# Kernel optimization log

Hardware: AMD Instinct MI355X
Metric: run time of the kernel (lower is better)

## Reference

```python
import jax, jax.numpy as jnp
import numpy as np

BITWIDTH = 8  # args.actBitwidth


def setup_inputs() -> dict:
    key = jax.random.key(0)
    k1, k2, k3 = jax.random.split(key, 3)
    x = jax.random.normal(k1, (32, 256, 56, 56), dtype=jnp.float32)
    # orthonormal-ish projection matrix (stand-in for PCA eigenvectors)
    u = jax.random.normal(k2, (256, 256), dtype=jnp.float32) / np.float32(np.sqrt(256.0))
    # positive per-channel clamp values
    clamp_val = jax.random.uniform(k3, (256,), dtype=jnp.float32) * 3.0 + 0.5
    return {"x": x, "u": u, "clamp_val": clamp_val}


def reference(x, u, clamp_val):
    N, C, H, W = x.shape
    x = jax.nn.relu(x)
    # [C, N*H*W] channel-major flatten (matches transpose(0,1).view(C,-1))
    im = jnp.transpose(x, (1, 0, 2, 3)).reshape(C, -1)
    mn = jnp.mean(im, axis=1, keepdims=True)
    im = im - mn
    # PCA projection
    p = u.T @ im  # [C, NHW]
    # per-channel symmetric clamp
    c = clamp_val[:, None]
    pq = jnp.clip(p, -c, c)
    # per-channel dynamic min/max uniform quantization (fused over channels)
    dmax = jnp.max(pq, axis=1, keepdims=True)
    dmin = jnp.min(pq, axis=1, keepdims=True)
    rng = dmax - dmin
    scale = (2.0 ** BITWIDTH - 1.0) / jnp.where(rng == 0, 1.0, rng)
    q = jnp.round((pq - dmin) * scale) / scale + dmin
    q = jnp.where(rng == 0, pq, q)
    # project back, re-center, add channel means
    out = u @ q
    out = out - jnp.mean(out, axis=1, keepdims=True) + mn
    return jnp.transpose(out.reshape(C, N, H, W), (1, 0, 2, 3))
```

## Files before the change

### kernel.cpp

```cpp
#include <hip/hip_runtime.h>
#include <hip/hip_bf16.h>
#include <stdint.h>

#define CH    256
#define HWsz  3136
#define NIMG  32
#define COLS  (NIMG * HWsz)
#define KB    32
#define TN    64
#define TILES (COLS / TN)
#define PBLK  2
#define NBINS 8
#define CHUNK (TN * 20)

typedef float  f32x4  __attribute__((ext_vector_type(4)));
typedef __bf16 bf16x8 __attribute__((ext_vector_type(8)));

struct Stats {
  float mnsum[NBINS][CH];
  float mn[CH];
  float poff[CH];
  float clF[CH];
  unsigned dminK[NBINS][CH];
  unsigned dmaxK[NBINS][CH];
  float dminF[CH];
  float scaleF[CH];
  float invF[CH];
  float qsum[CH];
  float corr[CH];
  unsigned short u_bf[CH * CH];
  unsigned short uT_bf[CH * CH];
};

__device__ __forceinline__ unsigned short f2bf(float f) {
  union { float f; unsigned u; } v; v.f = f;
  unsigned r = v.u + 0x7fffu + ((v.u >> 16) & 1u);
  return (unsigned short)(r >> 16);
}
__device__ __forceinline__ float bf2f(unsigned short b) {
  union { unsigned u; float f; } v; v.u = ((unsigned)b) << 16;
  return v.f;
}
__device__ __forceinline__ unsigned pack_bf2(float a, float b) {
  return (unsigned)f2bf(a) | ((unsigned)f2bf(b) << 16);
}
__device__ __forceinline__ unsigned fkey(float f) {
  unsigned u = __float_as_uint(f);
  return (u & 0x80000000u) ? ~u : (u | 0x80000000u);
}
__device__ __forceinline__ float funkey(unsigned k) {
  unsigned u = (k & 0x80000000u) ? (k & 0x7fffffffu) : ~k;
  return __uint_as_float(u);
}
__device__ __forceinline__ float clampf(float v, float c) {
  return fminf(fmaxf(v, -c), c);
}
__device__ __forceinline__ float dq(float v, float dmin, float sc, float inv) {
  return sc == 0.f ? v : fmaf(rintf((v - dmin) * sc), inv, dmin);
}

__global__ void k_init(const float* __restrict__ u, Stats* st) {
  int b = blockIdx.x, t = threadIdx.x;
  st->u_bf[b * CH + t]  = f2bf(u[b * CH + t]);
  st->uT_bf[b * CH + t] = f2bf(u[t * CH + b]);
  if (b < NBINS) {
    st->mnsum[b][t] = 0.f;
    st->dminK[b][t] = 0xFFFFFFFFu;
    st->dmaxK[b][t] = 0u;
  }
  if (b == 0) st->qsum[t] = 0.f;
}

__global__ __launch_bounds__(256) void k_gemm1(const float* __restrict__ x,
                                               Stats* __restrict__ st,
                                               unsigned* __restrict__ pq,
                                               long nstride) {
  __shared__ __align__(16) unsigned ldsU[8 * CHUNK];
  __shared__ float smin[CH];
  __shared__ float smax[CH];

  const int t = threadIdx.x;
  const int lane = t & 63, wv = t >> 6;
  const int g = t & 15, cpair = t >> 4;
  const int c2 = cpair & 3;
  const int q = lane >> 4, r15 = lane & 15;
  const int wsw = (((wv ^ ((g >> 1) & 3)) << 2) | c2);

  const int t0 = blockIdx.x * PBLK;
  const unsigned short* uT = st->uT_bf;

  smin[t] = 1e30f;
  smax[t] = -1e30f;

  f32x4 acc[4][4] = {};
  float4 rA[8], rB[8];
  float relp[8][2] = {};

  auto ldtile = [&](int tile) {
    const int n = tile / 49, hw0 = (tile % 49) * TN;
    const float* p0 = x + (size_t)n * CH * HWsz + (size_t)(2 * cpair) * HWsz + hw0 + 4 * g;
#pragma unroll
    for (int kc = 0; kc < 8; ++kc) {
      const float* p = p0 + (size_t)(kc * KB) * HWsz;
      rA[kc] = *(const float4*)p;
      rB[kc] = *(const float4*)(p + HWsz);
    }
  };
  auto stageall = [&]() {
#pragma unroll
    for (int kc = 0; kc < 8; ++kc) {
      const float a[4] = {fmaxf(rA[kc].x, 0.f), fmaxf(rA[kc].y, 0.f),
                          fmaxf(rA[kc].z, 0.f), fmaxf(rA[kc].w, 0.f)};
      const float b[4] = {fmaxf(rB[kc].x, 0.f), fmaxf(rB[kc].y, 0.f),
                          fmaxf(rB[kc].z, 0.f), fmaxf(rB[kc].w, 0.f)};
      relp[kc][0] += (a[0] + a[1]) + (a[2] + a[3]);
      relp[kc][1] += (b[0] + b[1]) + (b[2] + b[3]);
      unsigned* dst = ldsU + kc * CHUNK;
#pragma unroll
      for (int i = 0; i < 4; ++i)
        dst[(4 * g + i) * 20 + wsw] = pack_bf2(a[i], b[i]);
    }
  };
  auto epi = [&](int tile) {
    const int n = tile / 49, hw0 = (tile % 49) * TN;
#pragma unroll
    for (int mt = 0; mt < 4; ++mt) {
      const int kp0 = 32 * wv + 8 * mt + 2 * q;
      float mn4[4], mx4[4];
#pragma unroll
      for (int nt = 0; nt < 4; ++nt) {
        const unsigned w01 = pack_bf2(acc[mt][nt][0], acc[mt][nt][1]);
        const unsigned w23 = pack_bf2(acc[mt][nt][2], acc[mt][nt][3]);
        const size_t base = (size_t)n * nstride + (size_t)kp0 * HWsz + hw0 + nt * 16 + r15;
        pq[base]        = w01;
        pq[base + HWsz] = w23;
        const float v[4] = {bf2f((unsigned short)(w01 & 0xffffu)), bf2f((unsigned short)(w01 >> 16)),
                            bf2f((unsigned short)(w23 & 0xffffu)), bf2f((unsigned short)(w23 >> 16))};
#pragma unroll
        for (int reg = 0; reg < 4; ++reg) {
          if (nt == 0) { mn4[reg] = v[reg]; mx4[reg] = v[reg]; }
          else { mn4[reg] = fminf(mn4[reg], v[reg]); mx4[reg] = fmaxf(mx4[reg], v[reg]); }
        }
      }
#pragma unroll
      for (int reg = 0; reg < 4; ++reg) {
#pragma unroll
        for (int m = 8; m; m >>= 1) {
          mn4[reg] = fminf(mn4[reg], __shfl_xor(mn4[reg], m));
          mx4[reg] = fmaxf(mx4[reg], __shfl_xor(mx4[reg], m));
        }
        if (r15 == 0) {
          const int row = 64 * wv + 16 * mt + 4 * q + reg;
          smin[row] = fminf(smin[row], mn4[reg]);
          smax[row] = fmaxf(smax[row], mx4[reg]);
        }
      }
    }
  };

  ldtile(t0);

#pragma unroll
  for (int p = 0; p < PBLK; ++p) {
    __syncthreads();
    stageall();
    __syncthreads();
    if (p + 1 < PBLK) ldtile(t0 + p + 1);
#pragma unroll
    for (int kc = 0; kc < 8; ++kc) {
      bf16x8 afr[4];
#pragma unroll
      for (int mt = 0; mt < 4; ++mt)
        afr[mt] = *(const bf16x8*)(uT + (64 * wv + 16 * mt + r15) * CH + kc * KB + q * 8);
      bf16x8 bfr[4];
#pragma unroll
      for (int nt = 0; nt < 4; ++nt) {
        const int j = nt * 16 + r15;
        bfr[nt] = *(const bf16x8*)((const unsigned short*)(ldsU + kc * CHUNK) +
                                   (size_t)j * 40 + ((q ^ ((j >> 3) & 3)) << 3));
      }
#pragma unroll
      for (int nt = 0; nt < 4; ++nt)
#pragma unroll
        for (int mt = 0; mt < 4; ++mt)
          acc[mt][nt] = __builtin_amdgcn_mfma_f32_16x16x32_bf16(afr[mt], bfr[nt], acc[mt][nt], 0, 0, 0);
    }
    epi(t0 + p);
#pragma unroll
    for (int mt = 0; mt < 4; ++mt)
#pragma unroll
      for (int nt = 0; nt < 4; ++nt)
        acc[mt][nt] = (f32x4)(0.f);
  }

  __syncthreads();
  float (*scr)[17] = (float (*)[17])ldsU;
#pragma unroll
  for (int kc = 0; kc < 8; ++kc) {
    scr[kc * 32 + 2 * cpair + 0][g] = relp[kc][0];
    scr[kc * 32 + 2 * cpair + 1][g] = relp[kc][1];
  }
  __syncthreads();
  float s = 0.f;
#pragma unroll
  for (int i = 0; i < 16; ++i) s += scr[t][i];
  const int bin = blockIdx.x & (NBINS - 1);
  atomicAdd(&st->mnsum[bin][t], s);
  atomicMin(&st->dminK[bin][t], fkey(smin[t]));
  atomicMax(&st->dmaxK[bin][t], fkey(smax[t]));
}

__global__ void k_finalize(const float* __restrict__ u,
                           const float* __restrict__ clampv, Stats* st) {
  int t = threadIdx.x;
  __shared__ float smn[CH];
  float msum = 0.f;
  unsigned kmin = 0xFFFFFFFFu, kmax = 0u;
#pragma unroll
  for (int b = 0; b < NBINS; ++b) {
    msum += st->mnsum[b][t];
    unsigned a = st->dminK[b][t], z = st->dmaxK[b][t];
    kmin = (a < kmin) ? a : kmin;
    kmax = (z > kmax) ? z : kmax;
  }
  float mnv = msum * (1.f / COLS);
  st->mn[t] = mnv;
  smn[t] = mnv;
  __syncthreads();
  float acc = 0.f;
  for (int c = 0; c < CH; ++c) acc += u[c * CH + t] * smn[c];
  st->poff[t] = acc;
  float cv = clampv[t];
  st->clF[t] = cv;
  float dmin = clampf(funkey(kmin) - acc, cv);
  float dmax = clampf(funkey(kmax) - acc, cv);
  float rng = dmax - dmin;
  float sc = 0.f, iv = 0.f;
  if (rng != 0.f) { sc = 255.f / rng; iv = rng / 255.f; }
  st->dminF[t] = dmin; st->scaleF[t] = sc; st->invF[t] = iv;
}

__global__ __launch_bounds__(256) void k_qsum(const unsigned* __restrict__ pq,
                                              long nstride,
                                              Stats* __restrict__ st) {
  __shared__ float w4a[4], w4b[4];
  const int blk = blockIdx.x;
  const int n = blk >> 7, kp = blk & 127;
  const int r0 = 2 * kp, r1 = r0 + 1;
  const float p0 = st->poff[r0], c0 = st->clF[r0], d0 = st->dminF[r0],
              sc0 = st->scaleF[r0], i0 = st->invF[r0];
  const float p1 = st->poff[r1], c1 = st->clF[r1], d1 = st->dminF[r1],
              sc1 = st->scaleF[r1], i1 = st->invF[r1];
  const uint4* p = (const uint4*)(pq + (size_t)n * nstride + (size_t)kp * HWsz);
  float s0 = 0.f, s1 = 0.f;
  for (int i = threadIdx.x; i < HWsz / 4; i += 256) {
    const uint4 w = p[i];
    const unsigned ws[4] = {w.x, w.y, w.z, w.w};
#pragma unroll
    for (int k = 0; k < 4; ++k) {
      s0 += dq(clampf(bf2f((unsigned short)(ws[k] & 0xffffu)) - p0, c0), d0, sc0, i0);
      s1 += dq(clampf(bf2f((unsigned short)(ws[k] >> 16)) - p1, c1), d1, sc1, i1);
    }
  }
  for (int off = 32; off; off >>= 1) {
    s0 += __shfl_down(s0, off);
    s1 += __shfl_down(s1, off);
  }
  int lane = threadIdx.x & 63, wvi = threadIdx.x >> 6;
  if (!lane) { w4a[wvi] = s0; w4b[wvi] = s1; }
  __syncthreads();
  if (threadIdx.x == 0) {
    atomicAdd(&st->qsum[r0], (w4a[0] + w4a[1]) + (w4a[2] + w4a[3]));
    atomicAdd(&st->qsum[r1], (w4b[0] + w4b[1]) + (w4b[2] + w4b[3]));
  }
}

__global__ void k_corr(const float* __restrict__ u, Stats* st) {
  int t = threadIdx.x;
  __shared__ float qm[CH];
  qm[t] = st->qsum[t] * (1.f / COLS);
  __syncthreads();
  float acc = 0.f;
  for (int r = 0; r < CH; ++r) acc += u[t * CH + r] * qm[r];
  st->corr[t] = st->mn[t] - acc;
}

__global__ __launch_bounds__(256) void k_gemm2(const unsigned* __restrict__ pq,
                                               long nstride,
                                               Stats* __restrict__ st,
                                               float* __restrict__ out) {
  __shared__ __align__(16) unsigned ldsU[8 * CHUNK];
  __shared__ float pf[CH], cl[CH], dm[CH], sc[CH], iv[CH], co[CH];

  const int t = threadIdx.x;
  const int lane = t & 63, wv = t >> 6;
  const int g = t & 15, kpl = t >> 4;
  const int c2 = kpl & 3;
  const int q = lane >> 4, r15 = lane & 15;
  const int wsw = (((wv ^ ((g >> 1) & 3)) << 2) | c2);

  const int t0 = blockIdx.x * PBLK;
  const unsigned short* uA = st->u_bf;

  pf[t] = st->poff[t]; cl[t] = st->clF[t]; dm[t] = st->dminF[t];
  sc[t] = st->scaleF[t]; iv[t] = st->invF[t]; co[t] = st->corr[t];
  __syncthreads();

  f32x4 acc[4][4] = {};
  uint4 rW[8];

  auto ldtile = [&](int tile) {
    const int n = tile / 49, hw0 = (tile % 49) * TN;
    const unsigned* p0 = pq + (size_t)n * nstride + (size_t)kpl * HWsz + hw0 + 4 * g;
#pragma unroll
    for (int kc = 0; kc < 8; ++kc)
      rW[kc] = *(const uint4*)(p0 + (size_t)(kc * 16) * HWsz);
  };
  auto stageall = [&]() {
#pragma unroll
    for (int kc = 0; kc < 8; ++kc) {
      const int R0 = 2 * (kc * 16 + kpl);
      const float p0 = pf[R0],     q0 = cl[R0],     e0 = dm[R0],     s0 = sc[R0],     v0 = iv[R0];
      const float p1 = pf[R0 + 1], q1 = cl[R0 + 1], e1 = dm[R0 + 1], s1 = sc[R0 + 1], v1 = iv[R0 + 1];
      const unsigned ws[4] = {rW[kc].x, rW[kc].y, rW[kc].z, rW[kc].w};
      unsigned* dst = ldsU + kc * CHUNK;
#pragma unroll
      for (int i = 0; i < 4; ++i) {
        const float a = dq(clampf(bf2f((unsigned short)(ws[i] & 0xffffu)) - p0, q0), e0, s0, v0);
        const float b = dq(clampf(bf2f((unsigned short)(ws[i] >> 16)) - p1, q1), e1, s1, v1);
        dst[(4 * g + i) * 20 + wsw] = pack_bf2(a, b);
      }
    }
  };
  auto epi = [&](int tile) {
    const int n = tile / 49, hw0 = (tile % 49) * TN;
#pragma unroll
    for (int mt = 0; mt < 4; ++mt)
#pragma unroll
      for (int reg = 0; reg < 4; ++reg) {
        const int row = 64 * wv + 16 * mt + 4 * q + reg;
        const float cr = co[row];
        const size_t obase = ((size_t)n * CH + row) * HWsz + hw0;
#pragma unroll
        for (int nt = 0; nt < 4; ++nt)
          out[obase + nt * 16 + r15] = acc[mt][nt][reg] + cr;
      }
  };

  ldtile(t0);

#pragma unroll
  for (int p = 0; p < PBLK; ++p) {
    __syncthreads();
    stageall();
    __syncthreads();
    if (p + 1 < PBLK) ldtile(t0 + p + 1);
#pragma unroll
    for (int kc = 0; kc < 8; ++kc) {
      bf16x8 afr[4];
#pragma unroll
      for (int mt = 0; mt < 4; ++mt)
        afr[mt] = *(const bf16x8*)(uA + (64 * wv + 16 * mt + r15) * CH + kc * KB + q * 8);
      bf16x8 bfr[4];
#pragma unroll
      for (int nt = 0; nt < 4; ++nt) {
        const int j = nt * 16 + r15;
        bfr[nt] = *(const bf16x8*)((const unsigned short*)(ldsU + kc * CHUNK) +
                                   (size_t)j * 40 + ((q ^ ((j >> 3) & 3)) << 3));
      }
#pragma unroll
      for (int nt = 0; nt < 4; ++nt)
#pragma unroll
        for (int mt = 0; mt < 4; ++mt)
          acc[mt][nt] = __builtin_amdgcn_mfma_f32_16x16x32_bf16(afr[mt], bfr[nt], acc[mt][nt], 0, 0, 0);
    }
    epi(t0 + p);
#pragma unroll
    for (int mt = 0; mt < 4; ++mt)
#pragma unroll
      for (int nt = 0; nt < 4; ++nt)
        acc[mt][nt] = (f32x4)(0.f);
  }
}

extern "C" void kernel_launch(void* const* d_in, const int* in_sizes, int n_in,
                              void* d_out, int out_size, void* d_ws, size_t ws_size,
                              hipStream_t stream) {
  const float* x  = (const float*)d_in[0];
  const float* u  = (const float*)d_in[1];
  const float* cv = (const float*)d_in[2];
  float* out = (float*)d_out;
  Stats* st = (Stats*)d_ws;

  const size_t pq_off = (sizeof(Stats) + 255) & ~(size_t)255;
  const size_t pq_bytes = (size_t)NIMG * (CH / 2) * HWsz * 4;
  unsigned* pq;
  long nstride;
  if (ws_size >= pq_off + pq_bytes) {
    pq = (unsigned*)((char*)d_ws + pq_off);
    nstride = (long)(CH / 2) * HWsz;
  } else {
    pq = (unsigned*)d_out + (size_t)(CH / 2) * HWsz;
    nstride = (long)CH * HWsz;
  }

  const int gemm_blocks = TILES / PBLK;

  k_init<<<CH, CH, 0, stream>>>(u, st);
  k_gemm1<<<gemm_blocks, 256, 0, stream>>>(x, st, pq, nstride);
  k_finalize<<<1, CH, 0, stream>>>(u, cv, st);
  k_qsum<<<NIMG * (CH / 2), 256, 0, stream>>>(pq, nstride, st);
  k_corr<<<1, CH, 0, stream>>>(u, st);
  k_gemm2<<<gemm_blocks, 256, 0, stream>>>(pq, nstride, st, out);
}
```

Before: 323.2 us.

## Process one tile per block in both GEMMs with higher occupancy bounds

Both GEMM kernels drop the two-tile-per-block software prefetch loop and process a single 64-column tile per block, doubling the grid. Launch bounds now request four blocks per SM, and gemm1 loads its input in two half-batches to cut register pressure. The shared-memory min/max accumulators are replaced by direct global atomics per row, and gemm2 reads the correction term from global memory. The aim is to raise occupancy so latency is hidden by more resident waves rather than explicit prefetch, at the cost of more global atomics and losing the in-block load/compute overlap.

```diff
diff --git a/kernel.cpp b/kernel.cpp
--- a/kernel.cpp
+++ b/kernel.cpp
@@ -9,7 +9,6 @@
 #define KB    32
 #define TN    64
 #define TILES (COLS / TN)
-#define PBLK  2
 #define NBINS 8
 #define CHUNK (TN * 20)
 
@@ -71,13 +70,11 @@
   if (b == 0) st->qsum[t] = 0.f;
 }
 
-__global__ __launch_bounds__(256) void k_gemm1(const float* __restrict__ x,
-                                               Stats* __restrict__ st,
-                                               unsigned* __restrict__ pq,
-                                               long nstride) {
+__global__ __launch_bounds__(256, 4) void k_gemm1(const float* __restrict__ x,
+                                                  Stats* __restrict__ st,
+                                                  unsigned* __restrict__ pq,
+                                                  long nstride) {
   __shared__ __align__(16) unsigned ldsU[8 * CHUNK];
-  __shared__ float smin[CH];
-  __shared__ float smax[CH];
 
   const int t = threadIdx.x;
   const int lane = t & 63, wv = t >> 6;
@@ -86,111 +83,106 @@
   const int q = lane >> 4, r15 = lane & 15;
   const int wsw = (((wv ^ ((g >> 1) & 3)) << 2) | c2);
 
-  const int t0 = blockIdx.x * PBLK;
+  const int tile = blockIdx.x;
+  const int n = tile / 49, hw0 = (tile % 49) * TN;
   const unsigned short* uT = st->uT_bf;
-
-  smin[t] = 1e30f;
-  smax[t] = -1e30f;
-
-  f32x4 acc[4][4] = {};
-  float4 rA[8], rB[8];
+  const int bin = blockIdx.x & (NBINS - 1);
+
+  float4 rA[4], rB[4];
   float relp[8][2] = {};
 
-  auto ldtile = [&](int tile) {
-    const int n = tile / 49, hw0 = (tile % 49) * TN;
-    const float* p0 = x + (size_t)n * CH * HWsz + (size_t)(2 * cpair) * HWsz + hw0 + 4 * g;
-#pragma unroll
-    for (int kc = 0; kc < 8; ++kc) {
-      const float* p = p0 + (size_t)(kc * KB) * HWsz;
-      rA[kc] = *(const float4*)p;
-      rB[kc] = *(const float4*)(p + HWsz);
+  const float* pbase = x + (size_t)n * CH * HWsz + (size_t)(2 * cpair) * HWsz + hw0 + 4 * g;
+
+  auto ld4 = [&](int h) {
+#pragma unroll
+    for (int i = 0; i < 4; ++i) {
+      const float* p = pbase + (size_t)((4 * h + i) * KB) * HWsz;
+      rA[i] = *(const float4*)p;
+      rB[i] = *(const float4*)(p + HWsz);
     }
   };
-  auto stageall = [&]() {
-#pragma unroll
-    for (int kc = 0; kc < 8; ++kc) {
-      const float a[4] = {fmaxf(rA[kc].x, 0.f), fmaxf(rA[kc].y, 0.f),
-                          fmaxf(rA[kc].z, 0.f), fmaxf(rA[kc].w, 0.f)};
-      const float b[4] = {fmaxf(rB[kc].x, 0.f), fmaxf(rB[kc].y, 0.f),
-                          fmaxf(rB[kc].z, 0.f), fmaxf(rB[kc].w, 0.f)};
+  auto stage4 = [&](int h) {
+#pragma unroll
+    for (int i = 0; i < 4; ++i) {
+      const int kc = 4 * h + i;
+      const float a[4] = {fmaxf(rA[i].x, 0.f), fmaxf(rA[i].y, 0.f),
+                          fmaxf(rA[i].z, 0.f), fmaxf(rA[i].w, 0.f)};
+      const float b[4] = {fmaxf(rB[i].x, 0.f), fmaxf(rB[i].y, 0.f),
+                          fmaxf(rB[i].z, 0.f), fmaxf(rB[i].w, 0.f)};
       relp[kc][0] += (a[0] + a[1]) + (a[2] + a[3]);
       relp[kc][1] += (b[0] + b[1]) + (b[2] + b[3]);
       unsigned* dst = ldsU + kc * CHUNK;
 #pragma unroll
-      for (int i = 0; i < 4; ++i)
-        dst[(4 * g + i) * 20 + wsw] = pack_bf2(a[i], b[i]);
+      for (int j = 0; j < 4; ++j)
+        dst[(4 * g + j) * 20 + wsw] = pack_bf2(a[j], b[j]);
     }
   };
-  auto epi = [&](int tile) {
-    const int n = tile / 49, hw0 = (tile % 49) * TN;
-#pragma unroll
-    for (int mt = 0; mt < 4; ++mt) {
-      const int kp0 = 32 * wv + 8 * mt + 2 * q;
-      float mn4[4], mx4[4];
-#pragma unroll
-      for (int nt = 0; nt < 4; ++nt) {
-        const unsigned w01 = pack_bf2(acc[mt][nt][0], acc[mt][nt][1]);
-        const unsigned w23 = pack_bf2(acc[mt][nt][2], acc[mt][nt][3]);
-        const size_t base = (size_t)n * nstride + (size_t)kp0 * HWsz + hw0 + nt * 16 + r15;
-        pq[base]        = w01;
-        pq[base + HWsz] = w23;
-        const float v[4] = {bf2f((unsigned short)(w01 & 0xffffu)), bf2f((unsigned short)(w01 >> 16)),
-                            bf2f((unsigned short)(w23 & 0xffffu)), bf2f((unsigned short)(w23 >> 16))};
-#pragma unroll
-        for (int reg = 0; reg < 4; ++reg) {
-          if (nt == 0) { mn4[reg] = v[reg]; mx4[reg] = v[reg]; }
-          else { mn4[reg] = fminf(mn4[reg], v[reg]); mx4[reg] = fmaxf(mx4[reg], v[reg]); }
-        }
+
+  ld4(0);
+  stage4(0);
+  ld4(1);
+  stage4(1);
+  __syncthreads();
+
+  f32x4 acc[4][4];
+#pragma unroll
+  for (int mt = 0; mt < 4; ++mt)
+#pragma unroll
+    for (int nt = 0; nt < 4; ++nt)
+      acc[mt][nt] = (f32x4)(0.f);
+
+#pragma unroll
+  for (int kc = 0; kc < 8; ++kc) {
+    bf16x8 afr[4];
+#pragma unroll
+    for (int mt = 0; mt < 4; ++mt)
+      afr[mt] = *(const bf16x8*)(uT + (64 * wv + 16 * mt + r15) * CH + kc * KB + q * 8);
+    bf16x8 bfr[4];
+#pragma unroll
+    for (int nt = 0; nt < 4; ++nt) {
+      const int j = nt * 16 + r15;
+      bfr[nt] = *(const bf16x8*)((const unsigned short*)(ldsU + kc * CHUNK) +
+                                 (size_t)j * 40 + ((q ^ ((j >> 3) & 3)) << 3));
+    }
+#pragma unroll
+    for (int nt = 0; nt < 4; ++nt)
+#pragma unroll
+      for (int mt = 0; mt < 4; ++mt)
+        acc[mt][nt] = __builtin_amdgcn_mfma_f32_16x16x32_bf16(afr[mt], bfr[nt], acc[mt][nt], 0, 0, 0);
+  }
+
+#pragma unroll
+  for (int mt = 0; mt < 4; ++mt) {
+    const int kp0 = 32 * wv + 8 * mt + 2 * q;
+    float mn4[4], mx4[4];
+#pragma unroll
+    for (int nt = 0; nt < 4; ++nt) {
+      const unsigned w01 = pack_bf2(acc[mt][nt][0], acc[mt][nt][1]);
+      const unsigned w23 = pack_bf2(acc[mt][nt][2], acc[mt][nt][3]);
+      const size_t base = (size_t)n * nstride + (size_t)kp0 * HWsz + hw0 + nt * 16 + r15;
+      pq[base]        = w01;
+      pq[base + HWsz] = w23;
+      const float v[4] = {bf2f((unsigned short)(w01 & 0xffffu)), bf2f((unsigned short)(w01 >> 16)),
+                          bf2f((unsigned short)(w23 & 0xffffu)), bf2f((unsigned short)(w23 >> 16))};
+#pragma unroll
+      for (int reg = 0; reg < 4; ++reg) {
+        if (nt == 0) { mn4[reg] = v[reg]; mx4[reg] = v[reg]; }
+        else { mn4[reg] = fminf(mn4[reg], v[reg]); mx4[reg] = fmaxf(mx4[reg], v[reg]); }
       }
-#pragma unroll
-      for (int reg = 0; reg < 4; ++reg) {
-#pragma unroll
-        for (int m = 8; m; m >>= 1) {
-          mn4[reg] = fminf(mn4[reg], __shfl_xor(mn4[reg], m));
-          mx4[reg] = fmaxf(mx4[reg], __shfl_xor(mx4[reg], m));
-        }
-        if (r15 == 0) {
-          const int row = 64 * wv + 16 * mt + 4 * q + reg;
-          smin[row] = fminf(smin[row], mn4[reg]);
-          smax[row] = fmaxf(smax[row], mx4[reg]);
-        }
+    }
+#pragma unroll
+    for (int reg = 0; reg < 4; ++reg) {
+#pragma unroll
+      for (int m = 8; m; m >>= 1) {
+        mn4[reg] = fminf(mn4[reg], __shfl_xor(mn4[reg], m));
+        mx4[reg] = fmaxf(mx4[reg], __shfl_xor(mx4[reg], m));
       }
-    }
-  };
-
-  ldtile(t0);
-
-#pragma unroll
-  for (int p = 0; p < PBLK; ++p) {
-    __syncthreads();
-    stageall();
-    __syncthreads();
-    if (p + 1 < PBLK) ldtile(t0 + p + 1);
-#pragma unroll
-    for (int kc = 0; kc < 8; ++kc) {
-      bf16x8 afr[4];
-#pragma unroll
-      for (int mt = 0; mt < 4; ++mt)
-        afr[mt] = *(const bf16x8*)(uT + (64 * wv + 16 * mt + r15) * CH + kc * KB + q * 8);
-      bf16x8 bfr[4];
-#pragma unroll
-      for (int nt = 0; nt < 4; ++nt) {
-        const int j = nt * 16 + r15;
-        bfr[nt] = *(const bf16x8*)((const unsigned short*)(ldsU + kc * CHUNK) +
-                                   (size_t)j * 40 + ((q ^ ((j >> 3) & 3)) << 3));
+      if (r15 == 0) {
+        const int row = 64 * wv + 16 * mt + 4 * q + reg;
+        atomicMin(&st->dminK[bin][row], fkey(mn4[reg]));
+        atomicMax(&st->dmaxK[bin][row], fkey(mx4[reg]));
       }
-#pragma unroll
-      for (int nt = 0; nt < 4; ++nt)
-#pragma unroll
-        for (int mt = 0; mt < 4; ++mt)
-          acc[mt][nt] = __builtin_amdgcn_mfma_f32_16x16x32_bf16(afr[mt], bfr[nt], acc[mt][nt], 0, 0, 0);
-    }
-    epi(t0 + p);
-#pragma unroll
-    for (int mt = 0; mt < 4; ++mt)
-#pragma unroll
-      for (int nt = 0; nt < 4; ++nt)
-        acc[mt][nt] = (f32x4)(0.f);
+    }
   }
 
   __syncthreads();
@@ -204,10 +196,7 @@
   float s = 0.f;
 #pragma unroll
   for (int i = 0; i < 16; ++i) s += scr[t][i];
-  const int bin = blockIdx.x & (NBINS - 1);
   atomicAdd(&st->mnsum[bin][t], s);
-  atomicMin(&st->dminK[bin][t], fkey(smin[t]));
-  atomicMax(&st->dmaxK[bin][t], fkey(smax[t]));
 }
 
 __global__ void k_finalize(const float* __restrict__ u,
@@ -285,12 +274,12 @@
   st->corr[t] = st->mn[t] - acc;
 }
 
-__global__ __launch_bounds__(256) void k_gemm2(const unsigned* __restrict__ pq,
-                                               long nstride,
-                                               Stats* __restrict__ st,
-                                               float* __restrict__ out) {
+__global__ __launch_bounds__(256, 4) void k_gemm2(const unsigned* __restrict__ pq,
+                                                  long nstride,
+                                                  Stats* __restrict__ st,
+                                                  float* __restrict__ out) {
   __shared__ __align__(16) unsigned ldsU[8 * CHUNK];
-  __shared__ float pf[CH], cl[CH], dm[CH], sc[CH], iv[CH], co[CH];
+  __shared__ float pf[CH], cl[CH], dm[CH], sc[CH], iv[CH];
 
   const int t = threadIdx.x;
   const int lane = t & 63, wv = t >> 6;
@@ -299,88 +288,74 @@
   const int q = lane >> 4, r15 = lane & 15;
   const int wsw = (((wv ^ ((g >> 1) & 3)) << 2) | c2);
 
-  const int t0 = blockIdx.x * PBLK;
+  const int tile = blockIdx.x;
+  const int n = tile / 49, hw0 = (tile % 49) * TN;
   const unsigned short* uA = st->u_bf;
 
   pf[t] = st->poff[t]; cl[t] = st->clF[t]; dm[t] = st->dminF[t];
-  sc[t] = st->scaleF[t]; iv[t] = st->invF[t]; co[t] = st->corr[t];
-  __syncthreads();
-
-  f32x4 acc[4][4] = {};
+  sc[t] = st->scaleF[t]; iv[t] = st->invF[t];
+  __syncthreads();
+
   uint4 rW[8];
-
-  auto ldtile = [&](int tile) {
-    const int n = tile / 49, hw0 = (tile % 49) * TN;
-    const unsigned* p0 = pq + (size_t)n * nstride + (size_t)kpl * HWsz + hw0 + 4 * g;
-#pragma unroll
-    for (int kc = 0; kc < 8; ++kc)
-      rW[kc] = *(const uint4*)(p0 + (size_t)(kc * 16) * HWsz);
-  };
-  auto stageall = [&]() {
-#pragma unroll
-    for (int kc = 0; kc < 8; ++kc) {
-      const int R0 = 2 * (kc * 16 + kpl);
-      const float p0 = pf[R0],     q0 = cl[R0],     e0 = dm[R0],     s0 = sc[R0],     v0 = iv[R0];
-      const float p1 = pf[R0 + 1], q1 = cl[R0 + 1], e1 = dm[R0 + 1], s1 = sc[R0 + 1], v1 = iv[R0 + 1];
-      const unsigned ws[4] = {rW[kc].x, rW[kc].y, rW[kc].z, rW[kc].w};
-      unsigned* dst = ldsU + kc * CHUNK;
-#pragma unroll
-      for (int i = 0; i < 4; ++i) {
-        const float a = dq(clampf(bf2f((unsigned short)(ws[i] & 0xffffu)) - p0, q0), e0, s0, v0);
-        const float b = dq(clampf(bf2f((unsigned short)(ws[i] >> 16)) - p1, q1), e1, s1, v1);
-        dst[(4 * g + i) * 20 + wsw] = pack_bf2(a, b);
-      }
-    }
-  };
-  auto epi = [&](int tile) {
-    const int n = tile / 49, hw0 = (tile % 49) * TN;
+  const unsigned* p0g = pq + (size_t)n * nstride + (size_t)kpl * HWsz + hw0 + 4 * g;
+#pragma unroll
+  for (int kc = 0; kc < 8; ++kc)
+    rW[kc] = *(const uint4*)(p0g + (size_t)(kc * 16) * HWsz);
+
+#pragma unroll
+  for (int kc = 0; kc < 8; ++kc) {
+    const int R0 = 2 * (kc * 16 + kpl);
+    const float pp0 = pf[R0],     q0 = cl[R0],     e0 = dm[R0],     s0 = sc[R0],     v0 = iv[R0];
+    const float pp1 = pf[R0 + 1], q1 = cl[R0 + 1], e1 = dm[R0 + 1], s1 = sc[R0 + 1], v1 = iv[R0 + 1];
+    const unsigned ws[4] = {rW[kc].x, rW[kc].y, rW[kc].z, rW[kc].w};
+    unsigned* dst = ldsU + kc * CHUNK;
+#pragma unroll
+    for (int i = 0; i < 4; ++i) {
+      const float a = dq(clampf(bf2f((unsigned short)(ws[i] & 0xffffu)) - pp0, q0), e0, s0, v0);
+      const float b = dq(clampf(bf2f((unsigned short)(ws[i] >> 16)) - pp1, q1), e1, s1, v1);
+      dst[(4 * g + i) * 20 + wsw] = pack_bf2(a, b);
+    }
+  }
+  __syncthreads();
+
+  f32x4 acc[4][4];
+#pragma unroll
+  for (int mt = 0; mt < 4; ++mt)
+#pragma unroll
+    for (int nt = 0; nt < 4; ++nt)
+      acc[mt][nt] = (f32x4)(0.f);
+
+#pragma unroll
+  for (int kc = 0; kc < 8; ++kc) {
+    bf16x8 afr[4];
 #pragma unroll
     for (int mt = 0; mt < 4; ++mt)
-#pragma unroll
-      for (int reg = 0; reg < 4; ++reg) {
-        const int row = 64 * wv + 16 * mt + 4 * q + reg;
-        const float cr = co[row];
-        const size_t obase = ((size_t)n * CH + row) * HWsz + hw0;
-#pragma unroll
-        for (int nt = 0; nt < 4; ++nt)
-          out[obase + nt * 16 + r15] = acc[mt][nt][reg] + cr;
-      }
-  };
-
-  ldtile(t0);
-
-#pragma unroll
-  for (int p = 0; p < PBLK; ++p) {
-    __syncthreads();
-    stageall();
-    __syncthreads();
-    if (p + 1 < PBLK) ldtile(t0 + p + 1);
-#pragma unroll
-    for (int kc = 0; kc < 8; ++kc) {
-      bf16x8 afr[4];
+      afr[mt] = *(const bf16x8*)(uA + (64 * wv + 16 * mt + r15) * CH + kc * KB + q * 8);
+    bf16x8 bfr[4];
+#pragma unroll
+    for (int nt = 0; nt < 4; ++nt) {
+      const int j = nt * 16 + r15;
+      bfr[nt] = *(const bf16x8*)((const unsigned short*)(ldsU + kc * CHUNK) +
+                                 (size_t)j * 40 + ((q ^ ((j >> 3) & 3)) << 3));
+    }
+#pragma unroll
+    for (int nt = 0; nt < 4; ++nt)
 #pragma unroll
       for (int mt = 0; mt < 4; ++mt)
-        afr[mt] = *(const bf16x8*)(uA + (64 * wv + 16 * mt + r15) * CH + kc * KB + q * 8);
-      bf16x8 bfr[4];
-#pragma unroll
-      for (int nt = 0; nt < 4; ++nt) {
-        const int j = nt * 16 + r15;
-        bfr[nt] = *(const bf16x8*)((const unsigned short*)(ldsU + kc * CHUNK) +
-                                   (size_t)j * 40 + ((q ^ ((j >> 3) & 3)) << 3));
-      }
+        acc[mt][nt] = __builtin_amdgcn_mfma_f32_16x16x32_bf16(afr[mt], bfr[nt], acc[mt][nt], 0, 0, 0);
+  }
+
+#pragma unroll
+  for (int mt = 0; mt < 4; ++mt)
+#pragma unroll
+    for (int reg = 0; reg < 4; ++reg) {
+      const int row = 64 * wv + 16 * mt + 4 * q + reg;
+      const float cr = st->corr[row];
+      const size_t obase = ((size_t)n * CH + row) * HWsz + hw0;
 #pragma unroll
       for (int nt = 0; nt < 4; ++nt)
-#pragma unroll
-        for (int mt = 0; mt < 4; ++mt)
-          acc[mt][nt] = __builtin_amdgcn_mfma_f32_16x16x32_bf16(afr[mt], bfr[nt], acc[mt][nt], 0, 0, 0);
-    }
-    epi(t0 + p);
-#pragma unroll
-    for (int mt = 0; mt < 4; ++mt)
-#pragma unroll
-      for (int nt = 0; nt < 4; ++nt)
-        acc[mt][nt] = (f32x4)(0.f);
-  }
+        out[obase + nt * 16 + r15] = acc[mt][nt][reg] + cr;
+    }
 }
 
 extern "C" void kernel_launch(void* const* d_in, const int* in_sizes, int n_in,
@@ -404,12 +379,10 @@
     nstride = (long)CH * HWsz;
   }
 
-  const int gemm_blocks = TILES / PBLK;
-
   k_init<<<CH, CH, 0, stream>>>(u, st);
-  k_gemm1<<<gemm_blocks, 256, 0, stream>>>(x, st, pq, nstride);
+  k_gemm1<<<TILES, 256, 0, stream>>>(x, st, pq, nstride);
   k_finalize<<<1, CH, 0, stream>>>(u, cv, st);
   k_qsum<<<NIMG * (CH / 2), 256, 0, stream>>>(pq, nstride, st);
   k_corr<<<1, CH, 0, stream>>>(u, st);
-  k_gemm2<<<gemm_blocks, 256, 0, stream>>>(pq, nstride, st, out);
-}
+  k_gemm2<<<TILES, 256, 0, stream>>>(pq, nstride, st, out);
+}
```

Measured after the change: 322.7 us. About the same (-0.1%).
